# Kernel tuning notes

Measured on AMD Instinct MI355X. Metric: run time of the kernel, lower is better.

Reference implementation:

```python
import jax, jax.numpy as jnp
import numpy as np

NUM_EMBEDDINGS = 1024
EMBEDDING_DIM = 256


def setup_inputs() -> dict:
    key = jax.random.key(0)
    k1, k2 = jax.random.split(key)
    z = jax.random.normal(k1, (32, EMBEDDING_DIM, 32, 32), dtype=jnp.float32)
    codebook = jax.random.normal(k2, (NUM_EMBEDDINGS, EMBEDDING_DIM), dtype=jnp.float32)
    return {"z": z, "codebook": codebook}


def reference(z, codebook):
    # z: (B, C, H, W) -> (B, H, W, C) -> (B*H*W, C)
    B, C, H, W = z.shape
    z_bhwc = jnp.transpose(z, (0, 2, 3, 1))
    z_flat = z_bhwc.reshape(-1, C)  # (N, C)

    # pairwise squared distances: ||z||^2 + ||e||^2 - 2 z.e^T  -> (N, K)
    distances = (
        jnp.sum(z_flat ** 2, axis=1, keepdims=True)
        + jnp.sum(codebook ** 2, axis=1)
        - 2.0 * jnp.matmul(z_flat, codebook.T)
    )
    argmin_codewords = jnp.argmin(distances, axis=1)  # (N,)
    min_codewords = jax.nn.one_hot(argmin_codewords, NUM_EMBEDDINGS, dtype=jnp.float32)  # (N, K)

    # quantized latents via one-hot @ codebook, back to (B, C, H, W)
    z_quantized = jnp.matmul(min_codewords, codebook).reshape(B, H, W, C)
    z_quantized = jnp.transpose(z_quantized, (0, 3, 1, 2))
    return (min_codewords, z_quantized)
```

## Files before the change

### kernel.cpp

```cpp
#include <hip/hip_runtime.h>

#define N_ROWS 32768
#define K_CODES 1024
#define CDIM 256

typedef _Float16 half8 __attribute__((ext_vector_type(8)));
typedef _Float16 half4 __attribute__((ext_vector_type(4)));
typedef float floatx16 __attribute__((ext_vector_type(16)));
typedef unsigned long long ull;

#define WS_ZH   0ull
#define WS_ZL   16777216ull
#define WS_CBH  33554432ull
#define WS_CBL  34078720ull
#define WS_CBN  34603008ull
#define WS_PART 34607104ull
#define WS_IDX  36704256ull
#define WS_NEED 36835328ull

__device__ __forceinline__ void g2lds16(const void* g, void* l) {
    __builtin_amdgcn_global_load_lds(
        (const __attribute__((address_space(1))) void*)g,
        (__attribute__((address_space(3))) void*)l, 16, 0, 0);
}

__global__ __launch_bounds__(256) void prep_all(const float* __restrict__ z,
                                                const float* __restrict__ cb,
                                                _Float16* __restrict__ zh,
                                                _Float16* __restrict__ zl,
                                                _Float16* __restrict__ cbh,
                                                _Float16* __restrict__ cbl,
                                                float* __restrict__ cbn,
                                                ull* __restrict__ part) {
    __shared__ float t[64][68];
    if (blockIdx.x >= 2048) {
        int k = ((blockIdx.x - 2048) << 2) | (threadIdx.x >> 6);
        int lane = threadIdx.x & 63;
        float4 v = reinterpret_cast<const float4*>(cb + k * CDIM)[lane];
        float s0 = v.x * 32.f, s1 = v.y * 32.f, s2 = v.z * 32.f, s3 = v.w * 32.f;
        half4 hv, lv;
        hv[0] = (_Float16)s0; lv[0] = (_Float16)(s0 - (float)hv[0]);
        hv[1] = (_Float16)s1; lv[1] = (_Float16)(s1 - (float)hv[1]);
        hv[2] = (_Float16)s2; lv[2] = (_Float16)(s2 - (float)hv[2]);
        hv[3] = (_Float16)s3; lv[3] = (_Float16)(s3 - (float)hv[3]);
        size_t off = (size_t)((lane >> 1) * K_CODES + k) * 8 + ((lane & 1) * 4);
        *reinterpret_cast<half4*>(&cbh[off]) = hv;
        *reinterpret_cast<half4*>(&cbl[off]) = lv;
        float s = s0 * s0 + s1 * s1 + s2 * s2 + s3 * s3;
        #pragma unroll
        for (int off2 = 32; off2 > 0; off2 >>= 1) s += __shfl_down(s, off2);
        if (lane == 0) cbn[k] = s;
        return;
    }
    if (threadIdx.x < 16) part[blockIdx.x * 16 + threadIdx.x] = ~0ull;

    int hwt = blockIdx.x & 15;
    int ct  = (blockIdx.x >> 4) & 3;
    int bb  = blockIdx.x >> 6;
    int tid = threadIdx.x;
    #pragma unroll
    for (int p = 0; p < 4; p++) {
        int e = p * 256 + tid;
        int c = e >> 4, h4 = e & 15;
        float4 v = *reinterpret_cast<const float4*>(
            &z[((bb * 256 + ct * 64 + c) << 10) + hwt * 64 + h4 * 4]);
        *reinterpret_cast<float4*>(&t[c][h4 * 4]) = v;
    }
    __syncthreads();
    #pragma unroll
    for (int p = 0; p < 4; p++) {
        int e = p * 256 + tid;
        int hw = e >> 4, c4 = e & 15;
        half4 hv, lv;
        #pragma unroll
        for (int j = 0; j < 4; j++) {
            float s = t[c4 * 4 + j][hw] * 32.f;
            _Float16 h = (_Float16)s;
            hv[j] = h;
            lv[j] = (_Float16)(s - (float)h);
        }
        int n = bb * 1024 + hwt * 64 + hw;
        int cg = ct * 64 + c4 * 4;
        size_t off = (size_t)((cg >> 3) * N_ROWS + n) * 8 + (cg & 7);
        *reinterpret_cast<half4*>(&zh[off]) = hv;
        *reinterpret_cast<half4*>(&zl[off]) = lv;
    }
}

__global__ __launch_bounds__(256, 3) void vq_areg(
    const _Float16* __restrict__ zh, const _Float16* __restrict__ zl,
    const _Float16* __restrict__ cbh, const _Float16* __restrict__ cbl,
    const float* __restrict__ cbn, ull* __restrict__ part) {

    __shared__ _Float16 BhL[8192], BlL[8192];

    const int tid = threadIdx.x;
    const int lane = tid & 63, w = tid >> 6;
    const int fm = lane & 31, fq = lane >> 5;
    const int L = (blockIdx.x & 7) * 256 + (blockIdx.x >> 3);
    const int codeTile = L & 15;
    const int rowTile  = L >> 4;
    const int rowBase = rowTile * 256, codeBase = codeTile * 64;
    const int rw = rowBase + w * 64;

    auto stageB = [&](int h) {
        #pragma unroll
        for (int p = 0; p < 4; p++) {
            int G = p * 256 + tid;
            int plane = G >> 6, code = G & 63;
            size_t so = ((size_t)(h * 16 + plane) * K_CODES + codeBase + code) * 8;
            g2lds16(cbh + so, &BhL[G * 8]);
            g2lds16(cbl + so, &BlL[G * 8]);
        }
    };
    auto loadA = [&](int s, half8 (&h)[2], half8 (&l)[2]) {
        #pragma unroll
        for (int i = 0; i < 2; i++) {
            size_t ao = ((size_t)(2 * s + fq) * N_ROWS + rw + i * 32 + fm) * 8;
            h[i] = *reinterpret_cast<const half8*>(&zh[ao]);
            l[i] = *reinterpret_cast<const half8*>(&zl[ao]);
        }
    };

    float cbnv[2];
    #pragma unroll
    for (int j = 0; j < 2; j++) cbnv[j] = cbn[codeBase + j * 32 + fm];

    floatx16 acc[4];
    #pragma unroll
    for (int i = 0; i < 4; i++) acc[i] = (floatx16)0.f;

    half8 pah[2][2], pal[2][2];
    loadA(0, pah[0], pal[0]);
    stageB(0);
    __syncthreads();

    #pragma unroll
    for (int s = 0; s < 16; s++) {
        const int cur = s & 1, nxt = cur ^ 1;
        if (s == 8) {
            __syncthreads();
            stageB(1);
            __syncthreads();
        }
        if (s < 15) loadA(s + 1, pah[nxt], pal[nxt]);
        const int lp = (s & 7) * 2 + fq;
        half8 bh[2], bl[2];
        #pragma unroll
        for (int j = 0; j < 2; j++) {
            int gb = (lp * 64 + j * 32 + fm) * 8;
            bh[j] = *reinterpret_cast<const half8*>(&BhL[gb]);
            bl[j] = *reinterpret_cast<const half8*>(&BlL[gb]);
        }
        #pragma unroll
        for (int i = 0; i < 2; i++)
            #pragma unroll
            for (int j = 0; j < 2; j++) {
                acc[i*2+j] = __builtin_amdgcn_mfma_f32_32x32x16_f16(pah[cur][i], bh[j], acc[i*2+j], 0, 0, 0);
                acc[i*2+j] = __builtin_amdgcn_mfma_f32_32x32x16_f16(pal[cur][i], bh[j], acc[i*2+j], 0, 0, 0);
                acc[i*2+j] = __builtin_amdgcn_mfma_f32_32x32x16_f16(pah[cur][i], bl[j], acc[i*2+j], 0, 0, 0);
            }
    }

    #pragma unroll
    for (int i = 0; i < 2; i++)
        #pragma unroll
        for (int r = 0; r < 16; r++) {
            float best = 3.4e38f; int bcode = 0x7fffffff;
            #pragma unroll
            for (int j = 0; j < 2; j++) {
                float d = fmaf(-2.f, acc[i*2+j][r], cbnv[j]);
                int code = codeBase + j * 32 + fm;
                if (d < best) { best = d; bcode = code; }
            }
            #pragma unroll
            for (int m = 1; m < 32; m <<= 1) {
                float ov = __shfl_xor(best, m, 64);
                int   oc = __shfl_xor(bcode, m, 64);
                if (ov < best || (ov == best && oc < bcode)) { best = ov; bcode = oc; }
            }
            if (fm == 0) {
                int row = rw + i * 32 + (r & 3) + 8 * (r >> 2) + 4 * fq;
                unsigned u = __float_as_uint(best);
                u = (u & 0x80000000u) ? ~u : (u | 0x80000000u);
                atomicMin(&part[row], ((ull)u << 32) | (unsigned)bcode);
            }
        }
}

__global__ __launch_bounds__(256) void finalize(const ull* __restrict__ part,
                                                const float* __restrict__ cb,
                                                float* __restrict__ out0,
                                                float* __restrict__ out1) {
    const int tid = threadIdx.x;
    if (blockIdx.x < 2048) {
        __shared__ int sid[16];
        const int rb = blockIdx.x * 16;
        if (tid < 16) sid[tid] = (int)(part[rb + tid] & 0xffffffffu);
        __syncthreads();
        const int k4 = tid << 2;
        #pragma unroll
        for (int r = 0; r < 16; r++) {
            int id = sid[r];
            float4 v4;
            v4.x = (k4     == id) ? 1.f : 0.f;
            v4.y = (k4 + 1 == id) ? 1.f : 0.f;
            v4.z = (k4 + 2 == id) ? 1.f : 0.f;
            v4.w = (k4 + 3 == id) ? 1.f : 0.f;
            reinterpret_cast<float4*>(out0)[(size_t)(rb + r) * 256 + tid] = v4;
        }
        return;
    }
    __shared__ float tile[64][257];
    const int blk = blockIdx.x - 2048;
    const int n0 = (blk >> 2) << 8;
    const int c0 = (blk & 3) << 6;
    const int b  = n0 >> 10;
    const int hw0 = n0 & 1023;

    const int id = (int)(part[n0 + tid] & 0xffffffffu);
    const float4* cb4 = reinterpret_cast<const float4*>(cb);
    #pragma unroll
    for (int jj = 0; jj < 16; jj++) {
        float4 v = cb4[id * 64 + (c0 >> 2) + jj];
        tile[jj * 4 + 0][tid] = v.x;
        tile[jj * 4 + 1][tid] = v.y;
        tile[jj * 4 + 2][tid] = v.z;
        tile[jj * 4 + 3][tid] = v.w;
    }
    __syncthreads();
    #pragma unroll
    for (int c = 0; c < 64; c++) {
        out1[((size_t)(b * 256 + c0 + c) << 10) + hw0 + tid] = tile[c][tid];
    }
}


__global__ __launch_bounds__(64) void cb_norms(const float* __restrict__ cb,
                                               float* __restrict__ cbn) {
    int k = blockIdx.x;
    int lane = threadIdx.x;
    float4 v = reinterpret_cast<const float4*>(cb + k * CDIM)[lane];
    float s = v.x * v.x + v.y * v.y + v.z * v.z + v.w * v.w;
    #pragma unroll
    for (int off = 32; off > 0; off >>= 1) s += __shfl_down(s, off);
    if (lane == 0) cbn[k] = s;
}

__global__ __launch_bounds__(256) void cb_transpose(const float* __restrict__ cb,
                                                    float* __restrict__ cbt) {
    __shared__ float t[32][33];
    int k0 = (blockIdx.x & 31) * 32;
    int c0 = (blockIdx.x >> 5) * 32;
    int lane = threadIdx.x & 31;
    int row = threadIdx.x >> 5;
    #pragma unroll
    for (int s = 0; s < 4; s++) {
        int r = row + s * 8;
        t[r][lane] = cb[(k0 + r) * CDIM + c0 + lane];
    }
    __syncthreads();
    #pragma unroll
    for (int s = 0; s < 4; s++) {
        int r = row + s * 8;
        cbt[(c0 + r) * K_CODES + k0 + lane] = t[lane][r];
    }
}

__global__ __launch_bounds__(512, 2) void vq_argmin(const float* __restrict__ z,
                                                    const float* __restrict__ cbt,
                                                    const float* __restrict__ cbn,
                                                    int* __restrict__ idx_out) {
    __shared__ float As[64][128];
    __shared__ float Bs[64][256];

    const int tid = threadIdx.x;
    const int tx = tid & 31;
    const int ty = tid >> 5;
    const int rowBase = blockIdx.x * 128;
    const int bb = rowBase >> 10;
    const int hwBase = rowBase & 1023;

    float minv[8];
    int   mini[8];
    #pragma unroll
    for (int i = 0; i < 8; i++) { minv[i] = 3.4e38f; mini[i] = 0; }

    for (int kt = 0; kt < K_CODES; kt += 256) {
        float acc[2][2][4][4];
        #pragma unroll
        for (int a = 0; a < 2; a++)
            #pragma unroll
            for (int b = 0; b < 2; b++)
                #pragma unroll
                for (int i = 0; i < 4; i++)
                    #pragma unroll
                    for (int j = 0; j < 4; j++) acc[a][b][i][j] = 0.f;

        for (int ccb = 0; ccb < CDIM; ccb += 64) {
            #pragma unroll
            for (int l = 0; l < 4; l++) {
                int f = tid + l * 512;
                int r4 = f & 31, c = f >> 5;
                float4 v = *reinterpret_cast<const float4*>(
                    &z[((bb * 256 + ccb + c) << 10) + hwBase + r4 * 4]);
                *reinterpret_cast<float4*>(&As[c][r4 * 4]) = v;
            }
            #pragma unroll
            for (int l = 0; l < 8; l++) {
                int f = tid + l * 512;
                int k4 = f & 63, c = f >> 6;
                float4 v = *reinterpret_cast<const float4*>(
                    &cbt[(ccb + c) * K_CODES + kt + k4 * 4]);
                *reinterpret_cast<float4*>(&Bs[c][k4 * 4]) = v;
            }
            __syncthreads();
            #pragma unroll 4
            for (int c = 0; c < 64; c++) {
                float4 a0 = *reinterpret_cast<const float4*>(&As[c][ty * 4]);
                float4 a1 = *reinterpret_cast<const float4*>(&As[c][64 + ty * 4]);
                float4 b0 = *reinterpret_cast<const float4*>(&Bs[c][tx * 4]);
                float4 b1 = *reinterpret_cast<const float4*>(&Bs[c][128 + tx * 4]);
                float av[2][4] = {{a0.x, a0.y, a0.z, a0.w}, {a1.x, a1.y, a1.z, a1.w}};
                float bw[2][4] = {{b0.x, b0.y, b0.z, b0.w}, {b1.x, b1.y, b1.z, b1.w}};
                #pragma unroll
                for (int ri = 0; ri < 2; ri++)
                    #pragma unroll
                    for (int i = 0; i < 4; i++)
                        #pragma unroll
                        for (int ci = 0; ci < 2; ci++)
                            #pragma unroll
                            for (int j = 0; j < 4; j++)
                                acc[ri][ci][i][j] =
                                    fmaf(av[ri][i], bw[ci][j], acc[ri][ci][i][j]);
            }
            __syncthreads();
        }
        #pragma unroll
        for (int ci = 0; ci < 2; ci++)
            #pragma unroll
            for (int j = 0; j < 4; j++) {
                int code = kt + ci * 128 + tx * 4 + j;
                float nrm = cbn[code];
                #pragma unroll
                for (int ri = 0; ri < 2; ri++)
                    #pragma unroll
                    for (int i = 0; i < 4; i++) {
                        float d = fmaf(-2.f, acc[ri][ci][i][j], nrm);
                        int r = ri * 4 + i;
                        if (d < minv[r]) { minv[r] = d; mini[r] = code; }
                    }
            }
    }

    __syncthreads();
    float (*rv)[32] = reinterpret_cast<float(*)[32]>(&As[0][0]);
    int   (*rix)[32] = reinterpret_cast<int(*)[32]>(&As[32][0]);
    #pragma unroll
    for (int ri = 0; ri < 2; ri++)
        #pragma unroll
        for (int i = 0; i < 4; i++) {
            int row = ri * 64 + ty * 4 + i;
            rv[row][tx] = minv[ri * 4 + i];
            rix[row][tx] = mini[ri * 4 + i];
        }
    __syncthreads();
    if (tid < 128) {
        float bvv = rv[tid][0]; int bii = rix[tid][0];
        #pragma unroll
        for (int t = 1; t < 32; t++) {
            float v = rv[tid][t]; int ii = rix[tid][t];
            if (v < bvv || (v == bvv && ii < bii)) { bvv = v; bii = ii; }
        }
        idx_out[rowBase + tid] = bii;
    }
}

__global__ __launch_bounds__(256) void onehot_fill(const int* __restrict__ idx,
                                                   float* __restrict__ out) {
    int i = blockIdx.x * 256 + threadIdx.x;
    int n  = i >> 8;
    int k4 = (i & 255) << 2;
    int id = idx[n];
    float4 v;
    v.x = (k4     == id) ? 1.f : 0.f;
    v.y = (k4 + 1 == id) ? 1.f : 0.f;
    v.z = (k4 + 2 == id) ? 1.f : 0.f;
    v.w = (k4 + 3 == id) ? 1.f : 0.f;
    reinterpret_cast<float4*>(out)[i] = v;
}

__global__ __launch_bounds__(256) void zq_fill2(const int* __restrict__ idx,
                                                const float* __restrict__ cb,
                                                float* __restrict__ out) {
    __shared__ float tile[64][257];
    const int tid = threadIdx.x;
    const int n0 = (blockIdx.x >> 2) << 8;
    const int c0 = (blockIdx.x & 3) << 6;
    const int b  = n0 >> 10;
    const int hw0 = n0 & 1023;

    const int id = idx[n0 + tid];
    const float4* cb4 = reinterpret_cast<const float4*>(cb);
    #pragma unroll
    for (int jj = 0; jj < 16; jj++) {
        float4 v = cb4[id * 64 + (c0 >> 2) + jj];
        tile[jj * 4 + 0][tid] = v.x;
        tile[jj * 4 + 1][tid] = v.y;
        tile[jj * 4 + 2][tid] = v.z;
        tile[jj * 4 + 3][tid] = v.w;
    }
    __syncthreads();
    #pragma unroll
    for (int c = 0; c < 64; c++) {
        out[((size_t)(b * 256 + c0 + c) << 10) + hw0 + tid] = tile[c][tid];
    }
}

extern "C" void kernel_launch(void* const* d_in, const int* in_sizes, int n_in,
                              void* d_out, int out_size, void* d_ws, size_t ws_size,
                              hipStream_t stream) {
    const float* z  = (const float*)d_in[0];
    const float* cb = (const float*)d_in[1];
    float* out0 = (float*)d_out;
    float* out1 = out0 + (size_t)N_ROWS * K_CODES;

    if (ws_size >= WS_NEED) {
        _Float16* zh  = (_Float16*)((char*)d_ws + WS_ZH);
        _Float16* zl  = (_Float16*)((char*)d_ws + WS_ZL);
        _Float16* cbh = (_Float16*)((char*)d_ws + WS_CBH);
        _Float16* cbl = (_Float16*)((char*)d_ws + WS_CBL);
        float* cbn = (float*)((char*)d_ws + WS_CBN);
        ull* part = (ull*)((char*)d_ws + WS_PART);

        prep_all<<<2304, 256, 0, stream>>>(z, cb, zh, zl, cbh, cbl, cbn, part);
        vq_areg<<<2048, 256, 0, stream>>>(zh, zl, cbh, cbl, cbn, part);
        finalize<<<2560, 256, 0, stream>>>(part, cb, out0, out1);
    } else {
        float* cbn = (float*)d_ws;
        int*   idx = (int*)((char*)d_ws + 4096);
        float* cbt = (float*)((char*)d_ws + 4096 + 131072);

        cb_norms<<<K_CODES, 64, 0, stream>>>(cb, cbn);
        cb_transpose<<<256, 256, 0, stream>>>(cb, cbt);
        vq_argmin<<<N_ROWS / 128, 512, 0, stream>>>(z, cbt, cbn, idx);
        onehot_fill<<<(N_ROWS * K_CODES / 4) / 256, 256, 0, stream>>>(idx, out0);
        zq_fill2<<<512, 256, 0, stream>>>(idx, cb, out1);
    }
}
```

Baseline: 280.4 us.

## Fuse finalize into VQ kernel via last-block-per-row-tile counter

Removes the separate finalize kernel. Each VQ block increments a per-row-tile counter after its atomicMin updates, and the last of the 16 code-tile blocks for that row tile writes the one-hot rows and the quantized output directly. This drops one kernel launch and lets output writes overlap with the distance computation of other blocks. In exchange, the output writes fall on only 128 blocks, which may serialize the bandwidth-heavy tail, and the out1 writes are now scalar strided stores instead of the LDS-transposed coalesced stores.

```diff
diff --git a/kernel.cpp b/kernel.cpp
--- a/kernel.cpp
+++ b/kernel.cpp
@@ -15,7 +15,7 @@
 #define WS_CBL  34078720ull
 #define WS_CBN  34603008ull
 #define WS_PART 34607104ull
-#define WS_IDX  36704256ull
+#define WS_CNT  36704256ull
 #define WS_NEED 36835328ull
 
 __device__ __forceinline__ void g2lds16(const void* g, void* l) {
@@ -31,7 +31,8 @@
                                                 _Float16* __restrict__ cbh,
                                                 _Float16* __restrict__ cbl,
                                                 float* __restrict__ cbn,
-                                                ull* __restrict__ part) {
+                                                ull* __restrict__ part,
+                                                unsigned* __restrict__ cnt) {
     __shared__ float t[64][68];
     if (blockIdx.x >= 2048) {
         int k = ((blockIdx.x - 2048) << 2) | (threadIdx.x >> 6);
@@ -53,6 +54,7 @@
         return;
     }
     if (threadIdx.x < 16) part[blockIdx.x * 16 + threadIdx.x] = ~0ull;
+    if (blockIdx.x < 128 && threadIdx.x == 16) cnt[blockIdx.x] = 0u;
 
     int hwt = blockIdx.x & 15;
     int ct  = (blockIdx.x >> 4) & 3;
@@ -87,12 +89,16 @@
     }
 }
 
-__global__ __launch_bounds__(256, 3) void vq_areg(
+__global__ __launch_bounds__(256, 3) void vq_fused(
     const _Float16* __restrict__ zh, const _Float16* __restrict__ zl,
     const _Float16* __restrict__ cbh, const _Float16* __restrict__ cbl,
-    const float* __restrict__ cbn, ull* __restrict__ part) {
+    const float* __restrict__ cbn, const float* __restrict__ cb,
+    ull* __restrict__ part, unsigned* __restrict__ cnt,
+    float* __restrict__ out0, float* __restrict__ out1) {
 
     __shared__ _Float16 BhL[8192], BlL[8192];
+    __shared__ int ids[256];
+    __shared__ unsigned lastFlag;
 
     const int tid = threadIdx.x;
     const int lane = tid & 63, w = tid >> 6;
@@ -186,52 +192,44 @@
                 atomicMin(&part[row], ((ull)u << 32) | (unsigned)bcode);
             }
         }
-}
-
-__global__ __launch_bounds__(256) void finalize(const ull* __restrict__ part,
-                                                const float* __restrict__ cb,
-                                                float* __restrict__ out0,
-                                                float* __restrict__ out1) {
-    const int tid = threadIdx.x;
-    if (blockIdx.x < 2048) {
-        __shared__ int sid[16];
-        const int rb = blockIdx.x * 16;
-        if (tid < 16) sid[tid] = (int)(part[rb + tid] & 0xffffffffu);
-        __syncthreads();
-        const int k4 = tid << 2;
-        #pragma unroll
-        for (int r = 0; r < 16; r++) {
-            int id = sid[r];
-            float4 v4;
-            v4.x = (k4     == id) ? 1.f : 0.f;
-            v4.y = (k4 + 1 == id) ? 1.f : 0.f;
-            v4.z = (k4 + 2 == id) ? 1.f : 0.f;
-            v4.w = (k4 + 3 == id) ? 1.f : 0.f;
-            reinterpret_cast<float4*>(out0)[(size_t)(rb + r) * 256 + tid] = v4;
-        }
-        return;
-    }
-    __shared__ float tile[64][257];
-    const int blk = blockIdx.x - 2048;
-    const int n0 = (blk >> 2) << 8;
-    const int c0 = (blk & 3) << 6;
-    const int b  = n0 >> 10;
-    const int hw0 = n0 & 1023;
-
-    const int id = (int)(part[n0 + tid] & 0xffffffffu);
+
+    __syncthreads();
+    if (tid == 0) {
+        __threadfence();
+        lastFlag = (atomicAdd(&cnt[rowTile], 1u) == 15u) ? 1u : 0u;
+    }
+    __syncthreads();
+    if (!lastFlag) return;
+    __threadfence();
+
+    ull pv = atomicAdd(&part[rowBase + tid], 0ull);
+    const int id = (int)(pv & 0xffffffffu);
+    ids[tid] = id;
+    __syncthreads();
+
+    const int k4 = tid << 2;
+    #pragma unroll 4
+    for (int r = 0; r < 256; r++) {
+        int idr = ids[r];
+        float4 v4;
+        v4.x = (k4     == idr) ? 1.f : 0.f;
+        v4.y = (k4 + 1 == idr) ? 1.f : 0.f;
+        v4.z = (k4 + 2 == idr) ? 1.f : 0.f;
+        v4.w = (k4 + 3 == idr) ? 1.f : 0.f;
+        reinterpret_cast<float4*>(out0)[(size_t)(rowBase + r) * 256 + tid] = v4;
+    }
+
+    const int b  = rowBase >> 10;
+    const int hw = (rowBase & 1023) + tid;
     const float4* cb4 = reinterpret_cast<const float4*>(cb);
-    #pragma unroll
-    for (int jj = 0; jj < 16; jj++) {
-        float4 v = cb4[id * 64 + (c0 >> 2) + jj];
-        tile[jj * 4 + 0][tid] = v.x;
-        tile[jj * 4 + 1][tid] = v.y;
-        tile[jj * 4 + 2][tid] = v.z;
-        tile[jj * 4 + 3][tid] = v.w;
-    }
-    __syncthreads();
-    #pragma unroll
-    for (int c = 0; c < 64; c++) {
-        out1[((size_t)(b * 256 + c0 + c) << 10) + hw0 + tid] = tile[c][tid];
+    #pragma unroll 4
+    for (int j = 0; j < 64; j++) {
+        float4 v = cb4[id * 64 + j];
+        size_t base = ((size_t)((b * 256 + j * 4) << 10)) + hw;
+        out1[base       ] = v.x;
+        out1[base + 1024] = v.y;
+        out1[base + 2048] = v.z;
+        out1[base + 3072] = v.w;
     }
 }
 
@@ -432,10 +430,11 @@
         _Float16* cbl = (_Float16*)((char*)d_ws + WS_CBL);
         float* cbn = (float*)((char*)d_ws + WS_CBN);
         ull* part = (ull*)((char*)d_ws + WS_PART);
-
-        prep_all<<<2304, 256, 0, stream>>>(z, cb, zh, zl, cbh, cbl, cbn, part);
-        vq_areg<<<2048, 256, 0, stream>>>(zh, zl, cbh, cbl, cbn, part);
-        finalize<<<2560, 256, 0, stream>>>(part, cb, out0, out1);
+        unsigned* cnt = (unsigned*)((char*)d_ws + WS_CNT);
+
+        prep_all<<<2304, 256, 0, stream>>>(z, cb, zh, zl, cbh, cbl, cbn, part, cnt);
+        vq_fused<<<2048, 256, 0, stream>>>(zh, zl, cbh, cbl, cbn, cb, part, cnt,
+                                           out0, out1);
     } else {
         float* cbn = (float*)d_ws;
         int*   idx = (int*)((char*)d_ws + 4096);
```

New measurement: 582.3 us. 108% more time.
